# Performance work log

Hardware: AMD Instinct MI355X
Metric: run time of the kernel (lower is better)

## Reference

```python
import jax, jax.numpy as jnp
import numpy as np
import math

B, S, D, H = 4, 2048, 1024, 16
HD = D // H  # head dim = 64


def setup_inputs() -> dict:
    key = jax.random.key(0)
    ks = jax.random.split(key, 8)
    queries = jax.random.normal(ks[0], (B, S, D), dtype=jnp.float32)
    keys = jax.random.normal(ks[1], (B, S, D), dtype=jnp.float32)
    values = jax.random.normal(ks[2], (B, S, D), dtype=jnp.float32)
    valid_lens = jnp.maximum(jax.random.randint(ks[3], (B,), 0, S), 1).astype(jnp.int64)
    scale = 1.0 / math.sqrt(D)
    Wq = jax.random.normal(ks[4], (H, D, HD), dtype=jnp.float32) * scale
    Wk = jax.random.normal(ks[5], (H, D, HD), dtype=jnp.float32) * scale
    Wv = jax.random.normal(ks[6], (H, D, HD), dtype=jnp.float32) * scale
    Wo = jax.random.normal(ks[7], (H * HD, D), dtype=jnp.float32) * scale
    return {"queries": queries, "keys": keys, "values": values,
            "valid_lens": valid_lens, "Wq": Wq, "Wk": Wk, "Wv": Wv, "Wo": Wo}


def reference(queries, keys, values, valid_lens, Wq, Wk, Wv, Wo):
    # Per-head projections, batched over heads: [B,S,D] x [H,D,HD] -> [B,H,S,HD]
    q = jnp.einsum('bsd,hde->bhse', queries, Wq)
    k = jnp.einsum('bsd,hde->bhse', keys, Wk)
    v = jnp.einsum('bsd,hde->bhse', values, Wv)
    # Scaled dot-product scores: [B,H,S,S]
    scores = jnp.einsum('bhse,bhte->bhst', q, k) / jnp.sqrt(jnp.float32(HD))
    # Padding mask only (causal=False default in the torch forward)
    pad = jnp.arange(S)[None, :] >= valid_lens[:, None]  # [B,S] True = masked
    scores = jnp.where(pad[:, None, None, :], -jnp.inf, scores)
    attn = jax.nn.softmax(scores, axis=-1)
    out = jnp.einsum('bhst,bhte->bhse', attn, v)  # [B,H,S,HD]
    out = out.transpose(0, 2, 1, 3).reshape(q.shape[0], S, H * HD)  # concat heads
    return out @ Wo
```

## Files before the change

### kernel.cpp

```cpp
#include <hip/hip_runtime.h>
#include <hip/hip_bf16.h>

typedef __bf16 bf16;
typedef __attribute__((ext_vector_type(8))) __bf16 bf16x8;
typedef __attribute__((ext_vector_type(4))) float f32x4;

#define DEV __device__ __forceinline__

DEV float fexp2(float x) {
#if __has_builtin(__builtin_amdgcn_exp2f)
  return __builtin_amdgcn_exp2f(x);
#else
  return exp2f(x);
#endif
}

DEV void gload_lds16(const void* g, void* l) {
  __builtin_amdgcn_global_load_lds(
      (__attribute__((address_space(1))) void*)(g),
      (__attribute__((address_space(3))) void*)(l), 16, 0, 0);
}

template <int N>
DEV void waitvm() { asm volatile("s_waitcnt vmcnt(%0)" ::"n"(N) : "memory"); }
DEV void waitlgkm0() { asm volatile("s_waitcnt lgkmcnt(0)" ::: "memory"); }
DEV void fence() { asm volatile("" ::: "memory"); }
DEV void bar() { fence(); __builtin_amdgcn_s_barrier(); fence(); }

__global__ void k_cvt_w(const float* __restrict__ Wq, const float* __restrict__ Wk,
                        const float* __restrict__ Wv, const float* __restrict__ Wo,
                        bf16* __restrict__ WqkvT, bf16* __restrict__ WoT) {
  const int idx = blockIdx.x * blockDim.x + threadIdx.x;
  const int which = idx >> 20, r = idx & ((1 << 20) - 1);
  if (which < 3) {
    const float* W = which == 0 ? Wq : which == 1 ? Wk : Wv;
    const int d = r & 1023, n = r >> 10;
    float val = W[((size_t)(n >> 6) << 16) + (size_t)d * 64 + (n & 63)];
    if (which == 0) val *= 0.180336880f;
    WqkvT[((size_t)which << 20) + r] = (bf16)val;
  } else {
    const int kk = r & 1023, n = r >> 10;
    WoT[r] = (bf16)Wo[(size_t)kk * 1024 + n];
  }
}

DEV void stageA(const bf16* __restrict__ Am, bf16 (*lds)[64], int k0, int tid) {
  const int wv = tid >> 6;
#pragma unroll
  for (int l = 0; l < 2; ++l) {
    const int row = l * 64 + (tid >> 3);
    const int e = (((tid & 7) ^ (row & 7)) << 3);
    gload_lds16(Am + (size_t)row * 1024 + k0 + e,
                (char*)lds + l * 8192 + wv * 1024);
  }
}
DEV void stageBh(const bf16* __restrict__ Bt, bf16 (*lds)[64], int h, int k0, int tid) {
  const int wv = tid >> 6;
#pragma unroll
  for (int l = 0; l < 2; ++l) {
    const int row = h * 128 + l * 64 + (tid >> 3);
    const int e = (((tid & 7) ^ (row & 7)) << 3);
    gload_lds16(Bt + (size_t)row * 1024 + k0 + e,
                (char*)lds + h * 16384 + l * 8192 + wv * 1024);
  }
}
DEV bf16x8 ldsfrag(const bf16 (*lds)[64], int row, int kk, int lgrp) {
  const int ch = ((kk << 2) + lgrp) ^ (row & 7);
  return *reinterpret_cast<const bf16x8*>((const char*)&lds[row][0] + (ch << 4));
}

DEV void loadA_f32(const float* __restrict__ Am, int k0, int tid, float4 v[4]) {
#pragma unroll
  for (int l = 0; l < 2; ++l) {
    const int row = l * 64 + (tid >> 3);
    const float* src = Am + (size_t)row * 1024 + k0 + (tid & 7) * 8;
    v[l * 2] = *reinterpret_cast<const float4*>(src);
    v[l * 2 + 1] = *reinterpret_cast<const float4*>(src + 4);
  }
}
DEV void writeA_lds(bf16 (*lds)[64], int tid, const float4 v[4]) {
#pragma unroll
  for (int l = 0; l < 2; ++l) {
    const int row = l * 64 + (tid >> 3);
    const int ch = (tid & 7) ^ (row & 7);
    union { bf16 h[8]; bf16x8 v8; } u;
    const float* f = (const float*)&v[l * 2];
#pragma unroll
    for (int j = 0; j < 8; ++j) u.h[j] = (bf16)f[j];
    *reinterpret_cast<bf16x8*>((char*)&lds[row][0] + (ch << 4)) = u.v8;
  }
}

#define GEMM_KLOOP(Am, Bt, acc)                                               \
  stageA(Am, AsB[0], 0, tid);                                                 \
  stageBh(Bt, BsB[0], 0, 0, tid);                                             \
  stageBh(Bt, BsB[0], 1, 0, tid);                                             \
  stageBh(Bt, BsB[1], 0, 64, tid);                                            \
  stageBh(Bt, BsB[1], 1, 64, tid);                                            \
  waitvm<4>();                                                                \
  bar();                                                                      \
  int cur = 0;                                                                \
  for (int kt = 0; kt < NT; ++kt) {                                           \
    bf16x8 bfr[4][2], afr[2][2];                                              \
    _Pragma("unroll") for (int n = 0; n < 4; ++n)                             \
        _Pragma("unroll") for (int kk = 0; kk < 2; ++kk)                      \
            bfr[n][kk] = ldsfrag(BsB[cur], wn * 64 + n * 16 + lid, kk, lgrp); \
    _Pragma("unroll") for (int mi = 0; mi < 2; ++mi)                          \
        _Pragma("unroll") for (int kk = 0; kk < 2; ++kk)                      \
            afr[mi][kk] = ldsfrag(AsB[cur], wr * 64 + mi * 16 + lid, kk, lgrp); \
    if (kt + 1 < NT) stageA(Am, AsB[cur ^ 1], (kt + 1) * 64, tid);            \
    bar();                                                                    \
    __builtin_amdgcn_s_setprio(1);                                            \
    _Pragma("unroll") for (int mi = 0; mi < 2; ++mi)                          \
        _Pragma("unroll") for (int n = 0; n < 4; ++n)                         \
            _Pragma("unroll") for (int kk = 0; kk < 2; ++kk)                  \
                acc[mi][n] = __builtin_amdgcn_mfma_f32_16x16x32_bf16(         \
                    afr[mi][kk], bfr[n][kk], acc[mi][n], 0, 0, 0);            \
    __builtin_amdgcn_s_setprio(0);                                            \
    bar();                                                                    \
    _Pragma("unroll") for (int mi = 0; mi < 2; ++mi)                          \
        _Pragma("unroll") for (int kk = 0; kk < 2; ++kk)                      \
            afr[mi][kk] = ldsfrag(AsB[cur], wr * 64 + (2 + mi) * 16 + lid, kk, lgrp); \
    if (kt + 2 < NT) {                                                        \
      stageBh(Bt, BsB[cur], 0, (kt + 2) * 64, tid);                           \
      stageBh(Bt, BsB[cur], 1, (kt + 2) * 64, tid);                           \
    }                                                                         \
    bar();                                                                    \
    __builtin_amdgcn_s_setprio(1);                                            \
    _Pragma("unroll") for (int mi = 0; mi < 2; ++mi)                          \
        _Pragma("unroll") for (int n = 0; n < 4; ++n)                         \
            _Pragma("unroll") for (int kk = 0; kk < 2; ++kk)                  \
                acc[2 + mi][n] = __builtin_amdgcn_mfma_f32_16x16x32_bf16(     \
                    afr[mi][kk], bfr[n][kk], acc[2 + mi][n], 0, 0, 0);        \
    __builtin_amdgcn_s_setprio(0);                                            \
    if (kt < NT - 2) waitvm<4>();                                             \
    else if (kt == NT - 2) waitvm<0>();                                       \
    bar();                                                                    \
    cur ^= 1;                                                                 \
  }

__global__ __launch_bounds__(512, 2) void k_gemm_qkv(const float* __restrict__ qF,
                                                     const float* __restrict__ kF,
                                                     const float* __restrict__ vF,
                                                     const bf16* __restrict__ Wt,
                                                     bf16* __restrict__ Qh,
                                                     bf16* __restrict__ Kh,
                                                     bf16* __restrict__ Vt) {
  __shared__ __align__(16) bf16 AsB[2][128][64];
  __shared__ __align__(16) bf16 BsB[2][256][64];
  const int tid = threadIdx.x, lane = tid & 63, w = tid >> 6;
  const int lgrp = lane >> 4, lid = lane & 15;
  const int wr = w >> 2, wn = w & 3;
  const int bid0 = blockIdx.x;
  const int bid = (bid0 & 7) * 96 + (bid0 >> 3);
  const int proj = bid >> 8;
  const int local = bid & 255;
  const int mt = local >> 2, ntl = local & 3;
  const int m0 = mt * 128, n0 = ntl * 256;
  const float* A = proj == 0 ? qF : proj == 1 ? kF : vF;
  const float* Am = A + (size_t)m0 * 1024;
  const bf16* Bt = Wt + ((size_t)proj * 1024 + n0) * 1024;

  f32x4 acc[4][4] = {};
  constexpr int NT = 16;

  float4 areg[4];
  loadA_f32(Am, 0, tid, areg);
  stageBh(Bt, BsB[0], 0, 0, tid);
  stageBh(Bt, BsB[0], 1, 0, tid);
  stageBh(Bt, BsB[1], 0, 64, tid);
  stageBh(Bt, BsB[1], 1, 64, tid);
  waitvm<8>();
  writeA_lds(AsB[0], tid, areg);
  waitvm<4>();
  waitlgkm0();
  bar();

  int cur = 0;
  for (int kt = 0; kt < NT; ++kt) {
    bf16x8 bfr[4][2], afr[2][2];
#pragma unroll
    for (int n = 0; n < 4; ++n)
#pragma unroll
      for (int kk = 0; kk < 2; ++kk)
        bfr[n][kk] = ldsfrag(BsB[cur], wn * 64 + n * 16 + lid, kk, lgrp);
#pragma unroll
    for (int mi = 0; mi < 2; ++mi)
#pragma unroll
      for (int kk = 0; kk < 2; ++kk)
        afr[mi][kk] = ldsfrag(AsB[cur], wr * 64 + mi * 16 + lid, kk, lgrp);
    if (kt + 1 < NT) loadA_f32(Am, (kt + 1) * 64, tid, areg);
    bar();
    __builtin_amdgcn_s_setprio(1);
#pragma unroll
    for (int mi = 0; mi < 2; ++mi)
#pragma unroll
      for (int n = 0; n < 4; ++n)
#pragma unroll
        for (int kk = 0; kk < 2; ++kk)
          acc[mi][n] = __builtin_amdgcn_mfma_f32_16x16x32_bf16(
              afr[mi][kk], bfr[n][kk], acc[mi][n], 0, 0, 0);
    __builtin_amdgcn_s_setprio(0);
    bar();
#pragma unroll
    for (int mi = 0; mi < 2; ++mi)
#pragma unroll
      for (int kk = 0; kk < 2; ++kk)
        afr[mi][kk] = ldsfrag(AsB[cur], wr * 64 + (2 + mi) * 16 + lid, kk, lgrp);
    if (kt + 2 < NT) {
      stageBh(Bt, BsB[cur], 0, (kt + 2) * 64, tid);
      stageBh(Bt, BsB[cur], 1, (kt + 2) * 64, tid);
    }
    if (kt + 1 < NT) {
      if (kt + 2 < NT) waitvm<4>();
      else waitvm<0>();
      writeA_lds(AsB[cur ^ 1], tid, areg);
    }
    bar();
    __builtin_amdgcn_s_setprio(1);
#pragma unroll
    for (int mi = 0; mi < 2; ++mi)
#pragma unroll
      for (int n = 0; n < 4; ++n)
#pragma unroll
        for (int kk = 0; kk < 2; ++kk)
          acc[2 + mi][n] = __builtin_amdgcn_mfma_f32_16x16x32_bf16(
              afr[mi][kk], bfr[n][kk], acc[2 + mi][n], 0, 0, 0);
    __builtin_amdgcn_s_setprio(0);
    waitlgkm0();
    bar();
    cur ^= 1;
  }

  const int hh = (n0 >> 6) + wn;
  if (proj == 0) {
#pragma unroll
    for (int mm = 0; mm < 4; ++mm) {
      const int rowb = m0 + wr * 64 + mm * 16 + lgrp * 4;
      const int bb = rowb >> 11, s = rowb & 2047;
#pragma unroll
      for (int n = 0; n < 4; ++n) {
        const int e = n * 16 + lid;
        bf16* dst = Qh + (((size_t)bb * 16 + hh) * 2048 + s) * 64 + e;
#pragma unroll
        for (int r = 0; r < 4; ++r) dst[(size_t)r * 64] = (bf16)acc[mm][n][r];
      }
    }
  } else if (proj == 1) {
#pragma unroll
    for (int mm = 0; mm < 4; ++mm) {
      const int rowb = m0 + wr * 64 + mm * 16 + lgrp * 4;
      const int bb = rowb >> 11, s = rowb & 2047;
#pragma unroll
      for (int n = 0; n < 4; ++n) {
        const int e = n * 16 + lid;
#pragma unroll
        for (int r = 0; r < 4; ++r) {
          const int sr = s + r;
          Kh[(((size_t)bb * 16 + hh) * 2048 + sr) * 64 + (e ^ ((sr & 7) << 3))] =
              (bf16)acc[mm][n][r];
        }
      }
    }
  } else {
#pragma unroll
    for (int mm = 0; mm < 4; ++mm) {
      const int rowb = m0 + wr * 64 + mm * 16 + lgrp * 4;
      const int bb = rowb >> 11, s = rowb & 2047;
#pragma unroll
      for (int n = 0; n < 4; ++n) {
        const int e = n * 16 + lid;
        union { bf16 hv[4]; uint2 u; } tmp;
#pragma unroll
        for (int r = 0; r < 4; ++r) tmp.hv[r] = (bf16)acc[mm][n][r];
        bf16* dst = Vt + (((size_t)bb * 16 + hh) * 64 + e) * 2048 + (s ^ ((e & 7) << 3));
        *reinterpret_cast<uint2*>(dst) = tmp.u;
      }
    }
  }
}

__global__ __launch_bounds__(512, 2) void k_gemm_out8(const bf16* __restrict__ A,
                                                      const bf16* __restrict__ Wo,
                                                      float* __restrict__ C) {
  __shared__ __align__(16) bf16 AsB[2][128][64];
  __shared__ __align__(16) bf16 BsB[2][256][64];
  const int tid = threadIdx.x, lane = tid & 63, w = tid >> 6;
  const int lgrp = lane >> 4, lid = lane & 15;
  const int wr = w >> 2, wn = w & 3;
  const int bid0 = blockIdx.x;
  const int bid = (bid0 & 7) * 32 + (bid0 >> 3);
  const int mt = bid >> 2, ntl = bid & 3;
  const int m0 = mt * 128, n0 = ntl * 256;
  const bf16* Am = A + (size_t)m0 * 1024;
  const bf16* Bt = Wo + (size_t)n0 * 1024;

  f32x4 acc[4][4] = {};
  constexpr int NT = 16;
  GEMM_KLOOP(Am, Bt, acc)

#pragma unroll
  for (int mm = 0; mm < 4; ++mm) {
    const int rowb = m0 + wr * 64 + mm * 16 + lgrp * 4;
#pragma unroll
    for (int n = 0; n < 4; ++n) {
      const int col = n0 + wn * 64 + n * 16 + lid;
#pragma unroll
      for (int r = 0; r < 4; ++r)
        C[(size_t)(rowb + r) * 1024 + col] = acc[mm][n][r];
    }
  }
}

__global__ __launch_bounds__(256, 3) void k_flash(const bf16* __restrict__ Qh,
                                                  const bf16* __restrict__ Ksw,
                                                  const bf16* __restrict__ Vsw,
                                                  const int* __restrict__ valid,
                                                  bf16* __restrict__ Ob) {
  __shared__ __align__(16) char Ks[2][8192];
  __shared__ __align__(16) char Vs[2][8192];
  __shared__ __align__(16) char Plds[4][4096];
  const int tid = threadIdx.x, lane = tid & 63, w = tid >> 6;
  const int lgrp = lane >> 4, lid = lane & 15;
  const int blk = blockIdx.x;
  const int qt = blk & 15, bh = blk >> 4;
  const int b = bh >> 4, h = bh & 15;
  const int s0 = qt * 128 + w * 32;
  const bf16* Qp = Qh + ((size_t)bh * 2048 + s0) * 64;
  const bf16* Kp = Ksw + (size_t)bh * 2048 * 64;
  const bf16* Vp = Vsw + (size_t)bh * 64 * 2048;
  const int vl = valid[b];
  const int nt = (vl + 63) >> 6;
  const int full = vl >> 6;

  const int sr0 = 16 * w + (lane >> 3), col8 = (lane & 7) * 8;

  gload_lds16(Kp + (size_t)sr0 * 64 + col8, &Ks[0][(16 * w) * 128]);
  gload_lds16(Kp + (size_t)(sr0 + 8) * 64 + col8, &Ks[0][(16 * w + 8) * 128]);
  gload_lds16(Vp + (size_t)sr0 * 2048 + col8, &Vs[0][(16 * w) * 128]);
  gload_lds16(Vp + (size_t)(sr0 + 8) * 2048 + col8, &Vs[0][(16 * w + 8) * 128]);

  bf16x8 aq[2][2];
#pragma unroll
  for (int g = 0; g < 2; ++g)
#pragma unroll
    for (int c = 0; c < 2; ++c)
      aq[g][c] = *reinterpret_cast<const bf16x8*>(Qp + (g * 16 + lid) * 64 + c * 32 + lgrp * 8);

  f32x4 Of[2][4] = {};
  float mrow[2] = {-1e30f, -1e30f};
  float lpart[2] = {0.f, 0.f};
  char* Pw = &Plds[w][0];
  float* PwF = (float*)Pw;
  const int pswz = (lid & 7) << 4;

  int cur = 0;
  for (int t = 0; t < nt; ++t) {
    const int t0 = t * 64;
    __syncthreads();
    if (t + 1 < nt) {
      const int t1 = t0 + 64;
      gload_lds16(Kp + (size_t)(t1 + sr0) * 64 + col8, &Ks[cur ^ 1][(16 * w) * 128]);
      gload_lds16(Kp + (size_t)(t1 + sr0 + 8) * 64 + col8, &Ks[cur ^ 1][(16 * w + 8) * 128]);
      gload_lds16(Vp + (size_t)sr0 * 2048 + t1 + col8, &Vs[cur ^ 1][(16 * w) * 128]);
      gload_lds16(Vp + (size_t)(sr0 + 8) * 2048 + t1 + col8, &Vs[cur ^ 1][(16 * w + 8) * 128]);
    }
    f32x4 sc[2][4] = {{}, {}};
#pragma unroll
    for (int kk = 0; kk < 2; ++kk) {
      bf16x8 bkh[4];
#pragma unroll
      for (int ct = 0; ct < 4; ++ct) {
        const int row = ct * 16 + lid;
        bkh[ct] = *reinterpret_cast<const bf16x8*>(
            &Ks[cur][row * 128] + ((kk * 64 + lgrp * 16) ^ ((row & 7) << 4)));
      }
#pragma unroll
      for (int g = 0; g < 2; ++g)
#pragma unroll
        for (int ct = 0; ct < 4; ++ct)
          sc[g][ct] = __builtin_amdgcn_mfma_f32_16x16x32_bf16(bkh[ct], aq[g][kk],
                                                              sc[g][ct], 0, 0, 0);
    }
    if (t >= full) {
#pragma unroll
      for (int ct = 0; ct < 4; ++ct)
#pragma unroll
        for (int r = 0; r < 4; ++r) {
          const bool m = (t0 + ct * 16 + lgrp * 4 + r) >= vl;
          sc[0][ct][r] = m ? -1e30f : sc[0][ct][r];
          sc[1][ct][r] = m ? -1e30f : sc[1][ct][r];
        }
    }
    float vm[2];
#pragma unroll
    for (int g = 0; g < 2; ++g) {
      float v = fmaxf(fmaxf(fmaxf(sc[g][0][0], sc[g][0][1]), fmaxf(sc[g][0][2], sc[g][0][3])),
                      fmaxf(fmaxf(sc[g][1][0], sc[g][1][1]), fmaxf(sc[g][1][2], sc[g][1][3])));
      v = fmaxf(v, fmaxf(fmaxf(fmaxf(sc[g][2][0], sc[g][2][1]), fmaxf(sc[g][2][2], sc[g][2][3])),
                         fmaxf(fmaxf(sc[g][3][0], sc[g][3][1]), fmaxf(sc[g][3][2], sc[g][3][3]))));
      vm[g] = v;
    }
    if (__any((vm[0] > mrow[0] + 8.f) | (vm[1] > mrow[1] + 8.f))) {
#pragma unroll
      for (int g = 0; g < 2; ++g) {
        float v = vm[g];
        v = fmaxf(v, __shfl_xor(v, 16));
        v = fmaxf(v, __shfl_xor(v, 32));
        float mnew = fmaxf(mrow[g], v);
        float scl = fexp2(mrow[g] - mnew);
        mrow[g] = mnew;
        lpart[g] *= scl;
        if (lgrp == 0) PwF[g * 512 + lid] = scl;
      }
      asm volatile("s_waitcnt lgkmcnt(0)" ::: "memory");
      f32x4 sq0 = *reinterpret_cast<const f32x4*>(PwF + lgrp * 4);
      f32x4 sq1 = *reinterpret_cast<const f32x4*>(PwF + 512 + lgrp * 4);
#pragma unroll
      for (int f = 0; f < 4; ++f)
#pragma unroll
        for (int r = 0; r < 4; ++r) {
          Of[0][f][r] *= sq0[r];
          Of[1][f][r] *= sq1[r];
        }
    }
#pragma unroll
    for (int g = 0; g < 2; ++g)
#pragma unroll
      for (int ct = 0; ct < 4; ++ct)
#pragma unroll
        for (int r = 0; r < 4; ++r)
          sc[g][ct][r] = fexp2(sc[g][ct][r] - mrow[g]);
#pragma unroll
    for (int g = 0; g < 2; ++g)
#pragma unroll
      for (int ct = 0; ct < 4; ++ct) {
        union { bf16 hv[2]; unsigned int u; } p0, p1;
        p0.hv[0] = (bf16)sc[g][ct][0]; p0.hv[1] = (bf16)sc[g][ct][1];
        p1.hv[0] = (bf16)sc[g][ct][2]; p1.hv[1] = (bf16)sc[g][ct][3];
        char* base = Pw + g * 2048 + lid * 128 + ((ct * 32 + lgrp * 8) ^ pswz);
        *reinterpret_cast<unsigned int*>(base) = p0.u;
        *reinterpret_cast<unsigned int*>(base + 4) = p1.u;
      }
    asm volatile("s_waitcnt lgkmcnt(0)" ::: "memory");
    bf16x8 pa[2][2];
#pragma unroll
    for (int g = 0; g < 2; ++g) {
      pa[g][0] = *reinterpret_cast<const bf16x8*>(Pw + g * 2048 + lid * 128 + ((lgrp * 16) ^ pswz));
      pa[g][1] = *reinterpret_cast<const bf16x8*>(Pw + g * 2048 + lid * 128 + ((64 + lgrp * 16) ^ pswz));
    }
#pragma unroll
    for (int f = 0; f < 4; ++f) {
      const int row = f * 16 + lid;
      const char* vb = &Vs[cur][row * 128];
      const int msk = (row & 7) << 4;
      bf16x8 bv0 = *reinterpret_cast<const bf16x8*>(vb + ((lgrp * 16) ^ msk));
      bf16x8 bv1 = *reinterpret_cast<const bf16x8*>(vb + ((64 + lgrp * 16) ^ msk));
      Of[0][f] = __builtin_amdgcn_mfma_f32_16x16x32_bf16(pa[0][0], bv0, Of[0][f], 0, 0, 0);
      Of[0][f] = __builtin_amdgcn_mfma_f32_16x16x32_bf16(pa[0][1], bv1, Of[0][f], 0, 0, 0);
      Of[1][f] = __builtin_amdgcn_mfma_f32_16x16x32_bf16(pa[1][0], bv0, Of[1][f], 0, 0, 0);
      Of[1][f] = __builtin_amdgcn_mfma_f32_16x16x32_bf16(pa[1][1], bv1, Of[1][f], 0, 0, 0);
    }
#pragma unroll
    for (int g = 0; g < 2; ++g)
      lpart[g] += ((sc[g][0][0] + sc[g][0][1]) + (sc[g][0][2] + sc[g][0][3])) +
                  ((sc[g][1][0] + sc[g][1][1]) + (sc[g][1][2] + sc[g][1][3])) +
                  ((sc[g][2][0] + sc[g][2][1]) + (sc[g][2][2] + sc[g][2][3])) +
                  ((sc[g][3][0] + sc[g][3][1]) + (sc[g][3][2] + sc[g][3][3]));
    cur ^= 1;
  }
#pragma unroll
  for (int g = 0; g < 2; ++g) {
    float l = lpart[g];
    l += __shfl_xor(l, 16);
    l += __shfl_xor(l, 32);
    if (lgrp == 0) PwF[g * 512 + lid] = 1.f / l;
  }
  asm volatile("s_waitcnt lgkmcnt(0)" ::: "memory");
  f32x4 iq0 = *reinterpret_cast<const f32x4*>(PwF + lgrp * 4);
  f32x4 iq1 = *reinterpret_cast<const f32x4*>(PwF + 512 + lgrp * 4);
  bf16* Op = Ob + ((size_t)b * 2048 + s0) * 1024 + h * 64;
#pragma unroll
  for (int r = 0; r < 4; ++r)
#pragma unroll
    for (int f = 0; f < 4; ++f) {
      Op[(size_t)(lgrp * 4 + r) * 1024 + f * 16 + lid] = (bf16)(Of[0][f][r] * iq0[r]);
      Op[(size_t)(16 + lgrp * 4 + r) * 1024 + f * 16 + lid] = (bf16)(Of[1][f][r] * iq1[r]);
    }
}

extern "C" void kernel_launch(void* const* d_in, const int* in_sizes, int n_in,
                              void* d_out, int out_size, void* d_ws, size_t ws_size,
                              hipStream_t stream) {
  const float* q = (const float*)d_in[0];
  const float* k = (const float*)d_in[1];
  const float* v = (const float*)d_in[2];
  const int* vl = (const int*)d_in[3];
  const float* Wq = (const float*)d_in[4];
  const float* Wk = (const float*)d_in[5];
  const float* Wv = (const float*)d_in[6];
  const float* Wo = (const float*)d_in[7];

  char* ws = (char*)d_ws;
  const size_t SZW = (size_t)1024 * 1024 * 2;
  const size_t SZT = (size_t)8192 * 1024 * 2;
  bf16* WqkvT = (bf16*)(ws);
  bf16* WoT = (bf16*)(ws + 3 * SZW);
  bf16* Qh  = (bf16*)(ws + 4 * SZW);
  bf16* Kh  = (bf16*)(ws + 4 * SZW + SZT);
  bf16* Vt  = (bf16*)(ws + 4 * SZW + 2 * SZT);
  bf16* attnb = (bf16*)(ws + 4 * SZW + 3 * SZT);

  k_cvt_w<<<16384, 256, 0, stream>>>(Wq, Wk, Wv, Wo, WqkvT, WoT);
  k_gemm_qkv<<<768, 512, 0, stream>>>(q, k, v, WqkvT, Qh, Kh, Vt);
  k_flash<<<1024, 256, 0, stream>>>(Qh, Kh, Vt, vl, attnb);
  k_gemm_out8<<<256, 512, 0, stream>>>(attnb, WoT, (float*)d_out);
}
```

Baseline: 192.9 us.

## Stage fp32 activations directly into LDS and convert to bf16 on fragment load

The QKV projection GEMM now copies fp32 activation tiles straight into LDS with async global_load_lds instead of loading them into registers, converting to bf16 and writing LDS. The bf16 conversion moves to the fragment reads, and the vmcnt waits are restructured to match the new async pipeline. This removes the register round-trip and the extra LDS write and should shorten the critical path. In exchange, the A tile doubles in LDS (64KB), which forces launch_bounds down to one block per CU, and the conversion is now repeated on every fragment read.

```diff
diff --git a/kernel.cpp b/kernel.cpp
--- a/kernel.cpp
+++ b/kernel.cpp
@@ -23,7 +23,6 @@
 
 template <int N>
 DEV void waitvm() { asm volatile("s_waitcnt vmcnt(%0)" ::"n"(N) : "memory"); }
-DEV void waitlgkm0() { asm volatile("s_waitcnt lgkmcnt(0)" ::: "memory"); }
 DEV void fence() { asm volatile("" ::: "memory"); }
 DEV void bar() { fence(); __builtin_amdgcn_s_barrier(); fence(); }
 
@@ -54,6 +53,16 @@
                 (char*)lds + l * 8192 + wv * 1024);
   }
 }
+DEV void stageAf(const float* __restrict__ Am, float (*lds)[64], int k0, int tid) {
+  const int wv = tid >> 6;
+#pragma unroll
+  for (int l = 0; l < 4; ++l) {
+    const int row = l * 32 + (tid >> 4);
+    const int ch = (tid & 15) ^ (row & 15);
+    gload_lds16(Am + (size_t)row * 1024 + k0 + ch * 4,
+                (char*)lds + l * 8192 + wv * 1024);
+  }
+}
 DEV void stageBh(const bf16* __restrict__ Bt, bf16 (*lds)[64], int h, int k0, int tid) {
   const int wv = tid >> 6;
 #pragma unroll
@@ -68,27 +77,16 @@
   const int ch = ((kk << 2) + lgrp) ^ (row & 7);
   return *reinterpret_cast<const bf16x8*>((const char*)&lds[row][0] + (ch << 4));
 }
-
-DEV void loadA_f32(const float* __restrict__ Am, int k0, int tid, float4 v[4]) {
-#pragma unroll
-  for (int l = 0; l < 2; ++l) {
-    const int row = l * 64 + (tid >> 3);
-    const float* src = Am + (size_t)row * 1024 + k0 + (tid & 7) * 8;
-    v[l * 2] = *reinterpret_cast<const float4*>(src);
-    v[l * 2 + 1] = *reinterpret_cast<const float4*>(src + 4);
-  }
-}
-DEV void writeA_lds(bf16 (*lds)[64], int tid, const float4 v[4]) {
-#pragma unroll
-  for (int l = 0; l < 2; ++l) {
-    const int row = l * 64 + (tid >> 3);
-    const int ch = (tid & 7) ^ (row & 7);
-    union { bf16 h[8]; bf16x8 v8; } u;
-    const float* f = (const float*)&v[l * 2];
-#pragma unroll
-    for (int j = 0; j < 8; ++j) u.h[j] = (bf16)f[j];
-    *reinterpret_cast<bf16x8*>((char*)&lds[row][0] + (ch << 4)) = u.v8;
-  }
+DEV bf16x8 ldsfragAf(const float (*lds)[64], int row, int kk, int lgrp) {
+  const int s0 = (kk << 3) + (lgrp << 1);
+  const f32x4 a = *reinterpret_cast<const f32x4*>(
+      (const char*)&lds[row][0] + (((s0) ^ (row & 15)) << 4));
+  const f32x4 b = *reinterpret_cast<const f32x4*>(
+      (const char*)&lds[row][0] + (((s0 + 1) ^ (row & 15)) << 4));
+  bf16x8 o;
+  o[0] = (bf16)a[0]; o[1] = (bf16)a[1]; o[2] = (bf16)a[2]; o[3] = (bf16)a[3];
+  o[4] = (bf16)b[0]; o[5] = (bf16)b[1]; o[6] = (bf16)b[2]; o[7] = (bf16)b[3];
+  return o;
 }
 
 #define GEMM_KLOOP(Am, Bt, acc)                                               \
@@ -139,14 +137,14 @@
     cur ^= 1;                                                                 \
   }
 
-__global__ __launch_bounds__(512, 2) void k_gemm_qkv(const float* __restrict__ qF,
+__global__ __launch_bounds__(512, 1) void k_gemm_qkv(const float* __restrict__ qF,
                                                      const float* __restrict__ kF,
                                                      const float* __restrict__ vF,
                                                      const bf16* __restrict__ Wt,
                                                      bf16* __restrict__ Qh,
                                                      bf16* __restrict__ Kh,
                                                      bf16* __restrict__ Vt) {
-  __shared__ __align__(16) bf16 AsB[2][128][64];
+  __shared__ __align__(16) float AsF[2][128][64];
   __shared__ __align__(16) bf16 BsB[2][256][64];
   const int tid = threadIdx.x, lane = tid & 63, w = tid >> 6;
   const int lgrp = lane >> 4, lid = lane & 15;
@@ -164,16 +162,12 @@
   f32x4 acc[4][4] = {};
   constexpr int NT = 16;
 
-  float4 areg[4];
-  loadA_f32(Am, 0, tid, areg);
+  stageAf(Am, AsF[0], 0, tid);
   stageBh(Bt, BsB[0], 0, 0, tid);
   stageBh(Bt, BsB[0], 1, 0, tid);
   stageBh(Bt, BsB[1], 0, 64, tid);
   stageBh(Bt, BsB[1], 1, 64, tid);
-  waitvm<8>();
-  writeA_lds(AsB[0], tid, areg);
   waitvm<4>();
-  waitlgkm0();
   bar();
 
   int cur = 0;
@@ -188,8 +182,8 @@
     for (int mi = 0; mi < 2; ++mi)
 #pragma unroll
       for (int kk = 0; kk < 2; ++kk)
-        afr[mi][kk] = ldsfrag(AsB[cur], wr * 64 + mi * 16 + lid, kk, lgrp);
-    if (kt + 1 < NT) loadA_f32(Am, (kt + 1) * 64, tid, areg);
+        afr[mi][kk] = ldsfragAf(AsF[cur], wr * 64 + mi * 16 + lid, kk, lgrp);
+    if (kt + 1 < NT) stageAf(Am, AsF[cur ^ 1], (kt + 1) * 64, tid);
     bar();
     __builtin_amdgcn_s_setprio(1);
 #pragma unroll
@@ -206,15 +200,10 @@
     for (int mi = 0; mi < 2; ++mi)
 #pragma unroll
       for (int kk = 0; kk < 2; ++kk)
-        afr[mi][kk] = ldsfrag(AsB[cur], wr * 64 + (2 + mi) * 16 + lid, kk, lgrp);
+        afr[mi][kk] = ldsfragAf(AsF[cur], wr * 64 + (2 + mi) * 16 + lid, kk, lgrp);
     if (kt + 2 < NT) {
       stageBh(Bt, BsB[cur], 0, (kt + 2) * 64, tid);
       stageBh(Bt, BsB[cur], 1, (kt + 2) * 64, tid);
-    }
-    if (kt + 1 < NT) {
-      if (kt + 2 < NT) waitvm<4>();
-      else waitvm<0>();
-      writeA_lds(AsB[cur ^ 1], tid, areg);
     }
     bar();
     __builtin_amdgcn_s_setprio(1);
@@ -227,7 +216,8 @@
           acc[2 + mi][n] = __builtin_amdgcn_mfma_f32_16x16x32_bf16(
               afr[mi][kk], bfr[n][kk], acc[2 + mi][n], 0, 0, 0);
     __builtin_amdgcn_s_setprio(0);
-    waitlgkm0();
+    if (kt < NT - 2) waitvm<4>();
+    else if (kt == NT - 2) waitvm<0>();
     bar();
     cur ^= 1;
   }
```

Result: faster. 186.9 us (-3.1%).
